# Optimization experiments

Hardware: AMD Instinct MI355X
Metric: run time of the kernel (lower is better)

## Reference

```python
import jax, jax.numpy as jnp
import numpy as np

D_MODEL = 1024


def bitlinear(x, weight):
    # ternary quantization with straight-through estimator; forward value is w_q*scale
    scale = jnp.clip(jnp.mean(jnp.abs(weight), axis=1, keepdims=True), 1e-5, None)
    w_q = jnp.clip(jnp.round(weight / scale), -1.0, 1.0)
    w = weight + jax.lax.stop_gradient(w_q * scale - weight)
    return x @ w.T


def rmsnorm(x, w, eps=1e-6):
    return x * jax.lax.rsqrt(jnp.mean(x * x, axis=-1, keepdims=True) + eps) * w


def setup_inputs() -> dict:
    key = jax.random.key(0)
    ks = jax.random.split(key, 6)
    D = D_MODEL
    std = np.sqrt(2.0 / D)  # kaiming_normal fan_out
    return {
        "x": jax.random.normal(ks[0], (4, 4096, D), dtype=jnp.float32),
        "Wr": jax.random.normal(ks[1], (D, D), dtype=jnp.float32) * std,
        "Wk": jax.random.normal(ks[2], (D, D), dtype=jnp.float32) * std,
        "Wv": jax.random.normal(ks[3], (D, D), dtype=jnp.float32) * std,
        "Wo": jax.random.normal(ks[4], (D, D), dtype=jnp.float32) * std,
        "decay": jnp.ones((D,), dtype=jnp.float32) * 0.99,
        "ln_w": jnp.ones((D,), dtype=jnp.float32),
    }


def reference(x, Wr, Wk, Wv, Wo, decay, ln_w):
    B, T, D = x.shape
    r = jax.nn.sigmoid(bitlinear(x, Wr))
    k = bitlinear(x, Wk)
    v = bitlinear(x, Wv)
    dec = jax.nn.sigmoid(decay)                              # [D]
    kv = k * v                                               # [B,T,D]
    positions = jnp.arange(T, dtype=x.dtype)                 # [T]
    log_decay = jnp.log(jnp.clip(dec, 1e-7, None))           # [D]
    scale = jnp.exp(positions[:, None] * log_decay[None, :])  # [T,D]
    scaled = kv / jnp.clip(scale, 1e-10, None)[None]         # [B,T,D]
    cum = jnp.cumsum(scaled, axis=1)                         # [B,T,D]
    state = cum * scale[None]                                # [B,T,D]
    return bitlinear(rmsnorm(r * state, ln_w), Wo)
```

## Files before the change

### kernel.cpp

```cpp
#include <hip/hip_runtime.h>

typedef unsigned short u16;
typedef __attribute__((ext_vector_type(8))) short bf16x8;
typedef __attribute__((ext_vector_type(4))) float f32x4;
typedef __attribute__((ext_vector_type(4))) unsigned short u16x4;

#define DM 1024

__device__ __forceinline__ float bf2f(u16 u){
  union { unsigned int i; float f; } v; v.i = ((unsigned int)u)<<16; return v.f;
}
__device__ __forceinline__ u16 f2bf(float f){
  unsigned int x = __float_as_uint(f);
  return (u16)((x + 0x7FFFu + ((x>>16)&1u)) >> 16);
}

__global__ __launch_bounds__(256)
void quantize_w(const float* __restrict__ W0, const float* __restrict__ W1,
                const float* __restrict__ W2, const float* __restrict__ W3,
                u16* __restrict__ wq, float* __restrict__ wsc)
{
  const int gr   = blockIdx.x*4 + (threadIdx.x>>6);
  const int lane = threadIdx.x & 63;
  const int mat  = gr >> 10, row = gr & 1023;
  const float* W = (mat==0)?W0:(mat==1)?W1:(mat==2)?W2:W3;
  const float* wr = W + (size_t)row*DM;
  float4 v[4]; float s = 0.f;
  #pragma unroll
  for (int c=0;c<4;c++){
    v[c] = *(const float4*)&wr[c*256 + lane*4];
    s += fabsf(v[c].x)+fabsf(v[c].y)+fabsf(v[c].z)+fabsf(v[c].w);
  }
  #pragma unroll
  for (int off=32; off; off>>=1) s += __shfl_down(s, off);
  s = __shfl(s, 0);
  const float scale = fmaxf(s*(1.f/1024.f), 1e-5f);
  if (lane==0) wsc[gr] = scale;
  u16* wo = wq + (size_t)gr*DM;
  #pragma unroll
  for (int c=0;c<4;c++){
    u16x4 q;
    q[0] = f2bf(fminf(fmaxf(rintf(v[c].x/scale),-1.f),1.f));
    q[1] = f2bf(fminf(fmaxf(rintf(v[c].y/scale),-1.f),1.f));
    q[2] = f2bf(fminf(fmaxf(rintf(v[c].z/scale),-1.f),1.f));
    q[3] = f2bf(fminf(fmaxf(rintf(v[c].w/scale),-1.f),1.f));
    *(u16x4*)&wo[c*256 + lane*4] = q;
  }
}

__global__ void cvt_x(const float* __restrict__ x, u16* __restrict__ xb){
  const int i = (blockIdx.x*256 + threadIdx.x)*4;
  float4 v = *(const float4*)&x[i];
  u16x4 o; o[0]=f2bf(v.x); o[1]=f2bf(v.y); o[2]=f2bf(v.z); o[3]=f2bf(v.w);
  *(u16x4*)&xb[i] = o;
}


#define SB0 __builtin_amdgcn_sched_barrier(0)
#define WL4  do{ asm volatile("s_waitcnt lgkmcnt(4)" ::: "memory"); SB0; }while(0)
#define WL12 do{ asm volatile("s_waitcnt lgkmcnt(12)" ::: "memory"); SB0; }while(0)
#define WL0  do{ asm volatile("s_waitcnt lgkmcnt(0)" ::: "memory"); SB0; }while(0)
#define VM4  do{ asm volatile("s_waitcnt vmcnt(4)" ::: "memory"); SB0; }while(0)
#define VM0  do{ asm volatile("s_waitcnt vmcnt(0)" ::: "memory"); SB0; }while(0)
#define BARR do{ SB0; __builtin_amdgcn_s_barrier(); SB0; }while(0)

#define STG(gB, off, T, Q, buf) \
  __builtin_amdgcn_global_load_lds( \
    (const __attribute__((address_space(1))) void*)((const char*)(gB) + (off) + (Q)*131072 + (T)*128), \
    (__attribute__((address_space(3))) void*)((char*)(buf) + ldst + (Q)*8192), 16, 0, 0)

#define RD(base, off) (*(const bf16x8*)((const char*)(base) + (off)))

#define MFMA16(AF, B, MI) \
  __builtin_amdgcn_s_setprio(1); \
  _Pragma("unroll") \
  for (int ni=0; ni<4; ++ni){ \
    acc[MI][ni]   = __builtin_amdgcn_mfma_f32_16x16x32_bf16(AF[0], B[ni],   acc[MI][ni],   0,0,0); \
    acc[MI][ni]   = __builtin_amdgcn_mfma_f32_16x16x32_bf16(AF[1], B[4+ni], acc[MI][ni],   0,0,0); \
    acc[MI+1][ni] = __builtin_amdgcn_mfma_f32_16x16x32_bf16(AF[2], B[ni],   acc[MI+1][ni], 0,0,0); \
    acc[MI+1][ni] = __builtin_amdgcn_mfma_f32_16x16x32_bf16(AF[3], B[4+ni], acc[MI+1][ni], 0,0,0); \
  } \
  __builtin_amdgcn_s_setprio(0)

#define TILE(T, C, BCUR, BNXT) { \
  const char* la  = (const char*)sA[C]; \
  const char* lnA = (const char*)sA[(C)^1]; \
  const char* lnB = (const char*)sB[(C)^1]; \
   \
  ay[0]=RD(la, arow+2*2048+koff0); ay[1]=RD(la, arow+2*2048+koff1); \
  ay[2]=RD(la, arow+3*2048+koff0); ay[3]=RD(la, arow+3*2048+koff1); \
  if ((T)+1<nt){ STG(Ag, aoff, (T)+1, 0, sA[(C)^1]); STG(Ag, aoff, (T)+1, 1, sA[(C)^1]); \
                 STG(Ag, aoff, (T)+1, 2, sA[(C)^1]); STG(Ag, aoff, (T)+1, 3, sA[(C)^1]); } \
  WL4; MFMA16(ax, BCUR, 0); BARR; \
   \
  ax[0]=RD(la, arow+4*2048+koff0); ax[1]=RD(la, arow+4*2048+koff1); \
  ax[2]=RD(la, arow+5*2048+koff0); ax[3]=RD(la, arow+5*2048+koff1); \
  if ((T)+2<nt){ STG(Bg, boff, (T)+2, 0, sB[C]); STG(Bg, boff, (T)+2, 1, sB[C]); } \
  WL4; MFMA16(ay, BCUR, 2); BARR; \
   \
  ay[0]=RD(la, arow+6*2048+koff0); ay[1]=RD(la, arow+6*2048+koff1); \
  ay[2]=RD(la, arow+7*2048+koff0); ay[3]=RD(la, arow+7*2048+koff1); \
  if ((T)+2<nt){ STG(Bg, boff, (T)+2, 2, sB[C]); STG(Bg, boff, (T)+2, 3, sB[C]); } \
  WL4; MFMA16(ax, BCUR, 4); SB0; \
  if ((T)==nt-2) { VM0; } else if ((T)<nt-2) { VM4; } \
  BARR; \
   \
  if ((T)<nt-1){ \
    BNXT[0]=RD(lnB, brow+0*2048+koff0); BNXT[1]=RD(lnB, brow+1*2048+koff0); \
    BNXT[2]=RD(lnB, brow+2*2048+koff0); BNXT[3]=RD(lnB, brow+3*2048+koff0); \
    BNXT[4]=RD(lnB, brow+0*2048+koff1); BNXT[5]=RD(lnB, brow+1*2048+koff1); \
    BNXT[6]=RD(lnB, brow+2*2048+koff1); BNXT[7]=RD(lnB, brow+3*2048+koff1); \
    ax[0]=RD(lnA, arow+0*2048+koff0); ax[1]=RD(lnA, arow+0*2048+koff1); \
    ax[2]=RD(lnA, arow+1*2048+koff0); ax[3]=RD(lnA, arow+1*2048+koff1); \
    WL12; \
  } else { WL0; } \
  MFMA16(ay, BCUR, 6); BARR; \
}

template<int MODE>
__global__ __launch_bounds__(512, 2)
void gemm_p(const u16* __restrict__ Ag, const u16* __restrict__ Bg,
            const float* __restrict__ bscale,
            u16* __restrict__ o_r, u16* __restrict__ o_k, u16* __restrict__ o_v,
            float* __restrict__ o_f)
{
  __shared__ u16 sA[2][256*64];
  __shared__ u16 sB[2][256*64];
  const int tid = threadIdx.x, wave = tid>>6, lane = tid&63;
  const int lr = lane&15, lg = lane>>4;
  const int wm = wave>>2, wn = wave&3;
  const int bm0 = blockIdx.x*256, bn0 = blockIdx.y*256;
  constexpr int nt = 16;

  const int r8   = lane>>3;
  const int scol = ((lane&7)<<4) ^ (r8<<4);
  const size_t aoff = (size_t)(bm0 + wave*8 + r8)*2048 + scol;
  const size_t boff = (size_t)(bn0 + wave*8 + r8)*2048 + scol;
  const int ldst = wave*1024;
  const int S = (lr&7)<<4;
  const int koff0 = (0  + (lg<<4)) ^ S;
  const int koff1 = (64 + (lg<<4)) ^ S;
  const int arow = (wm*128 + lr)*128;
  const int brow = (wn*64  + lr)*128;

  f32x4 acc[8][4];
  #pragma unroll
  for (int i=0;i<8;i++)
    #pragma unroll
    for (int j=0;j<4;j++) acc[i][j] = (f32x4){0.f,0.f,0.f,0.f};

  bf16x8 bc[8], bn2[8], ax[4], ay[4];

  #pragma unroll
  for (int q=0;q<4;q++){ STG(Ag, aoff, 0, q, sA[0]); STG(Bg, boff, 0, q, sB[0]); }
  #pragma unroll
  for (int q=0;q<4;q++){ STG(Bg, boff, 1, q, sB[1]); }
  VM4;
  BARR;
  {
    const char* la0 = (const char*)sA[0];
    const char* lb0 = (const char*)sB[0];
    bc[0]=RD(lb0, brow+0*2048+koff0); bc[1]=RD(lb0, brow+1*2048+koff0);
    bc[2]=RD(lb0, brow+2*2048+koff0); bc[3]=RD(lb0, brow+3*2048+koff0);
    bc[4]=RD(lb0, brow+0*2048+koff1); bc[5]=RD(lb0, brow+1*2048+koff1);
    bc[6]=RD(lb0, brow+2*2048+koff1); bc[7]=RD(lb0, brow+3*2048+koff1);
    ax[0]=RD(la0, arow+0*2048+koff0); ax[1]=RD(la0, arow+0*2048+koff1);
    ax[2]=RD(la0, arow+1*2048+koff0); ax[3]=RD(la0, arow+1*2048+koff1);
  }
  for (int tp=0; tp<nt; tp+=2){
    TILE(tp,   0, bc, bn2)
    TILE(tp+1, 1, bn2, bc)
  }

  #pragma unroll
  for (int mi=0; mi<8; ++mi){
    #pragma unroll
    for (int ni=0; ni<4; ++ni){
      const int col = bn0 + wn*64 + ni*16 + lr;
      const float sc = bscale[col];
      const int rowb = bm0 + wm*128 + mi*16 + lg*4;
      const f32x4 a = acc[mi][ni];
      if (MODE==0){
        const int seg = col>>10, d = col&1023;
        #pragma unroll
        for (int r2=0;r2<4;r2++){
          const size_t o = (size_t)(rowb+r2)*DM + d;
          const float val = a[r2]*sc;
          if (seg==0)      o_r[o] = f2bf(1.f/(1.f+expf(-val)));
          else if (seg==1) o_k[o] = f2bf(val);
          else             o_v[o] = f2bf(val);
        }
      } else {
        #pragma unroll
        for (int r2=0;r2<4;r2++)
          o_f[(size_t)(rowb+r2)*DM + col] = a[r2]*sc;
      }
    }
  }
}

__global__ __launch_bounds__(256)
void kv_phase1(const u16* __restrict__ kb, const u16* __restrict__ vb,
               const float* __restrict__ decay, float* __restrict__ part)
{
  const int c = blockIdx.x & 127, b = blockIdx.x >> 7;
  const int d0 = threadIdx.x*4;
  float ld[4]; f32x4 sum = {0.f,0.f,0.f,0.f};
  #pragma unroll
  for (int j=0;j<4;j++){
    const float dec = 1.f/(1.f+expf(-decay[d0+j]));
    ld[j] = logf(fmaxf(dec, 1e-7f));
  }
  for (int t=c*32; t<c*32+32; ++t){
    const size_t base = ((size_t)(b*4096 + t))*DM + d0;
    const u16x4 k4 = *(const u16x4*)&kb[base];
    const u16x4 v4 = *(const u16x4*)&vb[base];
    const float tf = (float)t;
    #pragma unroll
    for (int j=0;j<4;j++){
      const float e = expf(tf*ld[j]);
      sum[j] += bf2f(k4[j])*bf2f(v4[j]) / fmaxf(e, 1e-10f);
    }
  }
  *(f32x4*)&part[((size_t)(b*128+c))*DM + d0] = sum;
}

__global__ void chunk_prefix(float* __restrict__ part){
  const int g = blockIdx.x*256 + threadIdx.x;
  const int b = g >> 8, d0 = (g & 255)*4;
  f32x4 run = {0.f,0.f,0.f,0.f};
  for (int c8=0; c8<128; c8+=8){
    f32x4 v[8];
    #pragma unroll
    for (int i=0;i<8;i++)
      v[i] = *(const f32x4*)&part[((size_t)(b*128+c8+i))*DM + d0];
    #pragma unroll
    for (int i=0;i<8;i++){
      const f32x4 tmp = v[i];
      *(f32x4*)&part[((size_t)(b*128+c8+i))*DM + d0] = run;
      run += tmp;
    }
  }
}

__global__ __launch_bounds__(256)
void scan_norm(const u16* __restrict__ kb, const u16* __restrict__ vb,
               const u16* __restrict__ rbuf, const float* __restrict__ part,
               const float* __restrict__ decay, const float* __restrict__ lnw,
               u16* __restrict__ yn)
{
  const int c = blockIdx.x & 127, b = blockIdx.x >> 7;
  const int tid = threadIdx.x, lane = tid&63, wave = tid>>6;
  const int d0 = tid*4;
  __shared__ float red[2][4];
  f32x4 run = *(const f32x4*)&part[((size_t)(b*128+c))*DM + d0];
  float ld[4], lw[4];
  #pragma unroll
  for (int j=0;j<4;j++){
    const float dec = 1.f/(1.f+expf(-decay[d0+j]));
    ld[j] = logf(fmaxf(dec, 1e-7f));
    lw[j] = lnw[d0+j];
  }
  for (int t=c*32; t<c*32+32; ++t){
    const size_t base = ((size_t)(b*4096+t))*DM + d0;
    const u16x4 k4 = *(const u16x4*)&kb[base];
    const u16x4 v4 = *(const u16x4*)&vb[base];
    const u16x4 r4 = *(const u16x4*)&rbuf[base];
    const float tf = (float)t;
    float y[4]; float ss = 0.f;
    #pragma unroll
    for (int j=0;j<4;j++){
      const float e = expf(tf*ld[j]);
      run[j] += bf2f(k4[j])*bf2f(v4[j]) / fmaxf(e, 1e-10f);
      const float st = run[j]*e;
      y[j] = bf2f(r4[j])*st;
      ss += y[j]*y[j];
    }
    #pragma unroll
    for (int off=32; off; off>>=1) ss += __shfl_down(ss, off);
    if (lane==0) red[t&1][wave] = ss;
    __builtin_amdgcn_s_barrier();
    const float tot = (red[t&1][0]+red[t&1][1])+(red[t&1][2]+red[t&1][3]);
    const float rs = 1.f/sqrtf(tot*(1.f/1024.f) + 1e-6f);
    u16x4 o;
    #pragma unroll
    for (int j=0;j<4;j++) o[j] = f2bf(y[j]*rs*lw[j]);
    *(u16x4*)&yn[base] = o;
  }
}

extern "C" void kernel_launch(void* const* d_in, const int* in_sizes, int n_in,
                              void* d_out, int out_size, void* d_ws, size_t ws_size,
                              hipStream_t stream)
{
  (void)in_sizes; (void)n_in; (void)out_size; (void)ws_size;
  const float* x    = (const float*)d_in[0];
  const float* Wr   = (const float*)d_in[1];
  const float* Wk   = (const float*)d_in[2];
  const float* Wv   = (const float*)d_in[3];
  const float* Wo   = (const float*)d_in[4];
  const float* dec  = (const float*)d_in[5];
  const float* lnw  = (const float*)d_in[6];

  char* ws = (char*)d_ws;
  u16*   wq     = (u16*)(ws + 0);
  float* wsc    = (float*)(ws + 8388608);
  u16*   rbuf   = (u16*)(ws + 8404992);
  u16*   kbuf   = (u16*)(ws + 41959424);
  u16*   vbuf   = (u16*)(ws + 75513856);
  float* part   = (float*)(ws + 109068288);
  u16*   xb     = (u16*)(ws + 111165440);
  u16*   yn     = xb;

  quantize_w<<<1024, 256, 0, stream>>>(Wr, Wk, Wv, Wo, wq, wsc);
  cvt_x<<<16384, 256, 0, stream>>>(x, xb);
  gemm_p<0><<<dim3(64,12), 512, 0, stream>>>(xb, wq, wsc, rbuf, kbuf, vbuf, nullptr);
  kv_phase1<<<512, 256, 0, stream>>>(kbuf, vbuf, dec, part);
  chunk_prefix<<<4, 256, 0, stream>>>(part);
  scan_norm<<<512, 256, 0, stream>>>(kbuf, vbuf, rbuf, part, dec, lnw, yn);
  gemm_p<1><<<dim3(64,4), 512, 0, stream>>>(yn, wq + 3*1024*1024, wsc + 3072,
                                            nullptr, nullptr, nullptr, (float*)d_out);
}
```

Baseline: 250.6 us.

## Switch GEMM inner loop to 32x32x16 bf16 MFMA with restructured LDS reads

Replaces the 16x16x32 MFMA tiling with 32x32x16 MFMA instructions, so each wave now holds 4x2 32x32 accumulator blocks. B fragments are re-read from LDS each tile instead of being prefetched into double-buffered registers, and A fragments rotate between two register sets. The main loop is split into a steady-state body without bounds checks plus two peeled tail tiles, and the epilogue is remapped to the 32x32 output layout. Larger MFMAs need fewer instructions and LDS fragment reads per FLOP, but B reads are no longer hidden behind the previous tile's compute, and the epilogue writes use a more scattered row pattern.

```diff
diff --git a/kernel.cpp b/kernel.cpp
--- a/kernel.cpp
+++ b/kernel.cpp
@@ -3,6 +3,7 @@
 typedef unsigned short u16;
 typedef __attribute__((ext_vector_type(8))) short bf16x8;
 typedef __attribute__((ext_vector_type(4))) float f32x4;
+typedef __attribute__((ext_vector_type(16))) float f32x16;
 typedef __attribute__((ext_vector_type(4))) unsigned short u16x4;
 
 #define DM 1024
@@ -58,7 +59,6 @@
 
 #define SB0 __builtin_amdgcn_sched_barrier(0)
 #define WL4  do{ asm volatile("s_waitcnt lgkmcnt(4)" ::: "memory"); SB0; }while(0)
-#define WL12 do{ asm volatile("s_waitcnt lgkmcnt(12)" ::: "memory"); SB0; }while(0)
 #define WL0  do{ asm volatile("s_waitcnt lgkmcnt(0)" ::: "memory"); SB0; }while(0)
 #define VM4  do{ asm volatile("s_waitcnt vmcnt(4)" ::: "memory"); SB0; }while(0)
 #define VM0  do{ asm volatile("s_waitcnt vmcnt(0)" ::: "memory"); SB0; }while(0)
@@ -66,55 +66,48 @@
 
 #define STG(gB, off, T, Q, buf) \
   __builtin_amdgcn_global_load_lds( \
-    (const __attribute__((address_space(1))) void*)((const char*)(gB) + (off) + (Q)*131072 + (T)*128), \
+    (const __attribute__((address_space(1))) void*)((const char*)(gB) + (off) + (Q)*131072 + (size_t)(T)*128), \
     (__attribute__((address_space(3))) void*)((char*)(buf) + ldst + (Q)*8192), 16, 0, 0)
 
 #define RD(base, off) (*(const bf16x8*)((const char*)(base) + (off)))
 
-#define MFMA16(AF, B, MI) \
+#define RDA4(DST, BASE, ROWOFF) \
+  DST[0]=RD(BASE,(ROWOFF)+koff0); DST[1]=RD(BASE,(ROWOFF)+koff1); \
+  DST[2]=RD(BASE,(ROWOFF)+koff2); DST[3]=RD(BASE,(ROWOFF)+koff3);
+
+#define MFMA8(AF, MI) \
   __builtin_amdgcn_s_setprio(1); \
   _Pragma("unroll") \
-  for (int ni=0; ni<4; ++ni){ \
-    acc[MI][ni]   = __builtin_amdgcn_mfma_f32_16x16x32_bf16(AF[0], B[ni],   acc[MI][ni],   0,0,0); \
-    acc[MI][ni]   = __builtin_amdgcn_mfma_f32_16x16x32_bf16(AF[1], B[4+ni], acc[MI][ni],   0,0,0); \
-    acc[MI+1][ni] = __builtin_amdgcn_mfma_f32_16x16x32_bf16(AF[2], B[ni],   acc[MI+1][ni], 0,0,0); \
-    acc[MI+1][ni] = __builtin_amdgcn_mfma_f32_16x16x32_bf16(AF[3], B[4+ni], acc[MI+1][ni], 0,0,0); \
+  for (int kk=0; kk<4; ++kk){ \
+    acc[MI][0] = __builtin_amdgcn_mfma_f32_32x32x16_bf16(AF[kk], bF[0][kk], acc[MI][0], 0,0,0); \
+    acc[MI][1] = __builtin_amdgcn_mfma_f32_32x32x16_bf16(AF[kk], bF[1][kk], acc[MI][1], 0,0,0); \
   } \
   __builtin_amdgcn_s_setprio(0)
 
-#define TILE(T, C, BCUR, BNXT) { \
+#define TILE(T, C, FULL) { \
   const char* la  = (const char*)sA[C]; \
+  const char* lb  = (const char*)sB[C]; \
   const char* lnA = (const char*)sA[(C)^1]; \
-  const char* lnB = (const char*)sB[(C)^1]; \
    \
-  ay[0]=RD(la, arow+2*2048+koff0); ay[1]=RD(la, arow+2*2048+koff1); \
-  ay[2]=RD(la, arow+3*2048+koff0); ay[3]=RD(la, arow+3*2048+koff1); \
-  if ((T)+1<nt){ STG(Ag, aoff, (T)+1, 0, sA[(C)^1]); STG(Ag, aoff, (T)+1, 1, sA[(C)^1]); \
-                 STG(Ag, aoff, (T)+1, 2, sA[(C)^1]); STG(Ag, aoff, (T)+1, 3, sA[(C)^1]); } \
-  WL4; MFMA16(ax, BCUR, 0); BARR; \
+  RDA4(bF[0], lb, brow) \
+  RDA4(bF[1], lb, brow+4096) \
+  RDA4(aA, la, arow+4096) \
+  if (FULL || (T)+1<nt){ STG(Ag,aoff,(T)+1,0,sA[(C)^1]); STG(Ag,aoff,(T)+1,1,sA[(C)^1]); \
+                         STG(Ag,aoff,(T)+1,2,sA[(C)^1]); STG(Ag,aoff,(T)+1,3,sA[(C)^1]); } \
+  WL4; MFMA8(aB, 0); BARR; \
    \
-  ax[0]=RD(la, arow+4*2048+koff0); ax[1]=RD(la, arow+4*2048+koff1); \
-  ax[2]=RD(la, arow+5*2048+koff0); ax[3]=RD(la, arow+5*2048+koff1); \
-  if ((T)+2<nt){ STG(Bg, boff, (T)+2, 0, sB[C]); STG(Bg, boff, (T)+2, 1, sB[C]); } \
-  WL4; MFMA16(ay, BCUR, 2); BARR; \
+  RDA4(aB, la, arow+2*4096) \
+  if (FULL || (T)+2<nt){ STG(Bg,boff,(T)+2,0,sB[C]); STG(Bg,boff,(T)+2,1,sB[C]); } \
+  WL4; MFMA8(aA, 1); BARR; \
    \
-  ay[0]=RD(la, arow+6*2048+koff0); ay[1]=RD(la, arow+6*2048+koff1); \
-  ay[2]=RD(la, arow+7*2048+koff0); ay[3]=RD(la, arow+7*2048+koff1); \
-  if ((T)+2<nt){ STG(Bg, boff, (T)+2, 2, sB[C]); STG(Bg, boff, (T)+2, 3, sB[C]); } \
-  WL4; MFMA16(ax, BCUR, 4); SB0; \
-  if ((T)==nt-2) { VM0; } else if ((T)<nt-2) { VM4; } \
+  RDA4(aA, la, arow+3*4096) \
+  if (FULL || (T)+2<nt){ STG(Bg,boff,(T)+2,2,sB[C]); STG(Bg,boff,(T)+2,3,sB[C]); } \
+  WL4; MFMA8(aB, 2); SB0; \
+  if (FULL || (T)<nt-2) { VM4; } else if ((T)==nt-2) { VM0; } \
   BARR; \
    \
-  if ((T)<nt-1){ \
-    BNXT[0]=RD(lnB, brow+0*2048+koff0); BNXT[1]=RD(lnB, brow+1*2048+koff0); \
-    BNXT[2]=RD(lnB, brow+2*2048+koff0); BNXT[3]=RD(lnB, brow+3*2048+koff0); \
-    BNXT[4]=RD(lnB, brow+0*2048+koff1); BNXT[5]=RD(lnB, brow+1*2048+koff1); \
-    BNXT[6]=RD(lnB, brow+2*2048+koff1); BNXT[7]=RD(lnB, brow+3*2048+koff1); \
-    ax[0]=RD(lnA, arow+0*2048+koff0); ax[1]=RD(lnA, arow+0*2048+koff1); \
-    ax[2]=RD(lnA, arow+1*2048+koff0); ax[3]=RD(lnA, arow+1*2048+koff1); \
-    WL12; \
-  } else { WL0; } \
-  MFMA16(ay, BCUR, 6); BARR; \
+  if (FULL || (T)<nt-1){ RDA4(aB, lnA, arow) WL4; } else { WL0; } \
+  MFMA8(aA, 3); BARR; \
 }
 
 template<int MODE>
@@ -127,7 +120,7 @@
   __shared__ u16 sA[2][256*64];
   __shared__ u16 sB[2][256*64];
   const int tid = threadIdx.x, wave = tid>>6, lane = tid&63;
-  const int lr = lane&15, lg = lane>>4;
+  const int ll = lane&31, lh = lane>>5;
   const int wm = wave>>2, wn = wave&3;
   const int bm0 = blockIdx.x*256, bn0 = blockIdx.y*256;
   constexpr int nt = 16;
@@ -137,19 +130,22 @@
   const size_t aoff = (size_t)(bm0 + wave*8 + r8)*2048 + scol;
   const size_t boff = (size_t)(bn0 + wave*8 + r8)*2048 + scol;
   const int ldst = wave*1024;
-  const int S = (lr&7)<<4;
-  const int koff0 = (0  + (lg<<4)) ^ S;
-  const int koff1 = (64 + (lg<<4)) ^ S;
-  const int arow = (wm*128 + lr)*128;
-  const int brow = (wn*64  + lr)*128;
-
-  f32x4 acc[8][4];
-  #pragma unroll
-  for (int i=0;i<8;i++)
-    #pragma unroll
-    for (int j=0;j<4;j++) acc[i][j] = (f32x4){0.f,0.f,0.f,0.f};
-
-  bf16x8 bc[8], bn2[8], ax[4], ay[4];
+  const int S = (ll&7)<<4;
+  const int koff0 = (0*32 + (lh<<4)) ^ S;
+  const int koff1 = (1*32 + (lh<<4)) ^ S;
+  const int koff2 = (2*32 + (lh<<4)) ^ S;
+  const int koff3 = (3*32 + (lh<<4)) ^ S;
+  const int arow = (wm*128 + ll)*128;
+  const int brow = (wn*64  + ll)*128;
+
+  f32x16 acc[4][2];
+  #pragma unroll
+  for (int i=0;i<4;i++)
+    #pragma unroll
+    for (int j=0;j<2;j++)
+      acc[i][j] = (f32x16){0,0,0,0,0,0,0,0,0,0,0,0,0,0,0,0};
+
+  bf16x8 bF[2][4], aA[4], aB[4];
 
   #pragma unroll
   for (int q=0;q<4;q++){ STG(Ag, aoff, 0, q, sA[0]); STG(Bg, boff, 0, q, sB[0]); }
@@ -157,43 +153,40 @@
   for (int q=0;q<4;q++){ STG(Bg, boff, 1, q, sB[1]); }
   VM4;
   BARR;
-  {
-    const char* la0 = (const char*)sA[0];
-    const char* lb0 = (const char*)sB[0];
-    bc[0]=RD(lb0, brow+0*2048+koff0); bc[1]=RD(lb0, brow+1*2048+koff0);
-    bc[2]=RD(lb0, brow+2*2048+koff0); bc[3]=RD(lb0, brow+3*2048+koff0);
-    bc[4]=RD(lb0, brow+0*2048+koff1); bc[5]=RD(lb0, brow+1*2048+koff1);
-    bc[6]=RD(lb0, brow+2*2048+koff1); bc[7]=RD(lb0, brow+3*2048+koff1);
-    ax[0]=RD(la0, arow+0*2048+koff0); ax[1]=RD(la0, arow+0*2048+koff1);
-    ax[2]=RD(la0, arow+1*2048+koff0); ax[3]=RD(la0, arow+1*2048+koff1);
-  }
-  for (int tp=0; tp<nt; tp+=2){
-    TILE(tp,   0, bc, bn2)
-    TILE(tp+1, 1, bn2, bc)
-  }
-
-  #pragma unroll
-  for (int mi=0; mi<8; ++mi){
-    #pragma unroll
-    for (int ni=0; ni<4; ++ni){
-      const int col = bn0 + wn*64 + ni*16 + lr;
+  RDA4(aB, (const char*)sA[0], arow)
+
+  for (int tp=0; tp<nt-2; tp+=2){
+    TILE(tp,   0, true)
+    TILE(tp+1, 1, true)
+  }
+  TILE(14, 0, false)
+  TILE(15, 1, false)
+
+  #pragma unroll
+  for (int m=0; m<4; ++m){
+    #pragma unroll
+    for (int n=0; n<2; ++n){
+      const int col = bn0 + wn*64 + n*32 + ll;
       const float sc = bscale[col];
-      const int rowb = bm0 + wm*128 + mi*16 + lg*4;
-      const f32x4 a = acc[mi][ni];
+      const int rowb = bm0 + wm*128 + m*32 + lh*4;
+      const f32x16 a = acc[m][n];
       if (MODE==0){
         const int seg = col>>10, d = col&1023;
         #pragma unroll
-        for (int r2=0;r2<4;r2++){
-          const size_t o = (size_t)(rowb+r2)*DM + d;
-          const float val = a[r2]*sc;
+        for (int r=0;r<16;r++){
+          const int row = rowb + (r&3) + 8*(r>>2);
+          const float val = a[r]*sc;
+          const size_t o = (size_t)row*DM + d;
           if (seg==0)      o_r[o] = f2bf(1.f/(1.f+expf(-val)));
           else if (seg==1) o_k[o] = f2bf(val);
           else             o_v[o] = f2bf(val);
         }
       } else {
         #pragma unroll
-        for (int r2=0;r2<4;r2++)
-          o_f[(size_t)(rowb+r2)*DM + col] = a[r2]*sc;
+        for (int r=0;r<16;r++){
+          const int row = rowb + (r&3) + 8*(r>>2);
+          o_f[(size_t)row*DM + col] = a[r]*sc;
+        }
       }
     }
   }
```

Measured after the change: 466.1 us. 1.86x slower.

## Replace 256x256 GEMM with 128x128 tiles loading B directly into registers

Applied to the files above, without the earlier changes.

Replaces the 512-thread 256x256-tile GEMM and its hand-scheduled software pipeline with a 256-thread 128x128-tile kernel. Only A is staged through LDS, double-buffered. B fragments are read straight from global memory into registers, skipping LDS staging for the weights. The aim is more resident blocks per CU (launch bounds 256,3), a larger grid and a simpler schedule. In exchange, data reuse per tile is lower, more global traffic goes to the weights, and the deeper interleaving of LDS reads with MFMA is lost.

```diff
diff --git a/kernel.cpp b/kernel.cpp
--- a/kernel.cpp
+++ b/kernel.cpp
@@ -57,128 +57,97 @@
 
 
 #define SB0 __builtin_amdgcn_sched_barrier(0)
-#define WL4  do{ asm volatile("s_waitcnt lgkmcnt(4)" ::: "memory"); SB0; }while(0)
-#define WL12 do{ asm volatile("s_waitcnt lgkmcnt(12)" ::: "memory"); SB0; }while(0)
-#define WL0  do{ asm volatile("s_waitcnt lgkmcnt(0)" ::: "memory"); SB0; }while(0)
-#define VM4  do{ asm volatile("s_waitcnt vmcnt(4)" ::: "memory"); SB0; }while(0)
-#define VM0  do{ asm volatile("s_waitcnt vmcnt(0)" ::: "memory"); SB0; }while(0)
 #define BARR do{ SB0; __builtin_amdgcn_s_barrier(); SB0; }while(0)
-
-#define STG(gB, off, T, Q, buf) \
-  __builtin_amdgcn_global_load_lds( \
-    (const __attribute__((address_space(1))) void*)((const char*)(gB) + (off) + (Q)*131072 + (T)*128), \
-    (__attribute__((address_space(3))) void*)((char*)(buf) + ldst + (Q)*8192), 16, 0, 0)
-
 #define RD(base, off) (*(const bf16x8*)((const char*)(base) + (off)))
 
-#define MFMA16(AF, B, MI) \
+#define ASTG(T, BUF) { _Pragma("unroll") \
+  for (int q=0;q<4;q++) \
+    __builtin_amdgcn_global_load_lds( \
+      (const __attribute__((address_space(1))) void*)(asrc[q] + (size_t)(T)*128), \
+      (__attribute__((address_space(3))) void*)((char*)(BUF) + ldst + q*4096), 16, 0, 0); }
+
+#define GBODY(T, C, DO_STAGE, WA, WB, TRAIL) { \
+  bf16x8 b0[4], b1[4], a0[4], a1[4]; \
+  _Pragma("unroll") \
+  for (int n=0;n<4;n++){ b0[n]=RD(bptr[n], (size_t)(T)*128); \
+                         b1[n]=RD(bptr[n], (size_t)(T)*128+64); } \
+  SB0; \
+  if (DO_STAGE) ASTG((T)+1, sA[(C)^1]); \
+  SB0; \
+  asm volatile("s_waitcnt vmcnt(" #WA ")" ::: "memory"); \
+  __builtin_amdgcn_s_barrier(); \
+  SB0; \
+  _Pragma("unroll") \
+  for (int m=0;m<4;m++){ a0[m]=RD((const char*)sA[C], arow + m*2048 + koff0); \
+                         a1[m]=RD((const char*)sA[C], arow + m*2048 + koff1); } \
+  SB0; \
+  asm volatile("s_waitcnt vmcnt(" #WB ") lgkmcnt(0)" ::: "memory"); \
+  SB0; \
   __builtin_amdgcn_s_setprio(1); \
   _Pragma("unroll") \
-  for (int ni=0; ni<4; ++ni){ \
-    acc[MI][ni]   = __builtin_amdgcn_mfma_f32_16x16x32_bf16(AF[0], B[ni],   acc[MI][ni],   0,0,0); \
-    acc[MI][ni]   = __builtin_amdgcn_mfma_f32_16x16x32_bf16(AF[1], B[4+ni], acc[MI][ni],   0,0,0); \
-    acc[MI+1][ni] = __builtin_amdgcn_mfma_f32_16x16x32_bf16(AF[2], B[ni],   acc[MI+1][ni], 0,0,0); \
-    acc[MI+1][ni] = __builtin_amdgcn_mfma_f32_16x16x32_bf16(AF[3], B[4+ni], acc[MI+1][ni], 0,0,0); \
-  } \
-  __builtin_amdgcn_s_setprio(0)
-
-#define TILE(T, C, BCUR, BNXT) { \
-  const char* la  = (const char*)sA[C]; \
-  const char* lnA = (const char*)sA[(C)^1]; \
-  const char* lnB = (const char*)sB[(C)^1]; \
-   \
-  ay[0]=RD(la, arow+2*2048+koff0); ay[1]=RD(la, arow+2*2048+koff1); \
-  ay[2]=RD(la, arow+3*2048+koff0); ay[3]=RD(la, arow+3*2048+koff1); \
-  if ((T)+1<nt){ STG(Ag, aoff, (T)+1, 0, sA[(C)^1]); STG(Ag, aoff, (T)+1, 1, sA[(C)^1]); \
-                 STG(Ag, aoff, (T)+1, 2, sA[(C)^1]); STG(Ag, aoff, (T)+1, 3, sA[(C)^1]); } \
-  WL4; MFMA16(ax, BCUR, 0); BARR; \
-   \
-  ax[0]=RD(la, arow+4*2048+koff0); ax[1]=RD(la, arow+4*2048+koff1); \
-  ax[2]=RD(la, arow+5*2048+koff0); ax[3]=RD(la, arow+5*2048+koff1); \
-  if ((T)+2<nt){ STG(Bg, boff, (T)+2, 0, sB[C]); STG(Bg, boff, (T)+2, 1, sB[C]); } \
-  WL4; MFMA16(ay, BCUR, 2); BARR; \
-   \
-  ay[0]=RD(la, arow+6*2048+koff0); ay[1]=RD(la, arow+6*2048+koff1); \
-  ay[2]=RD(la, arow+7*2048+koff0); ay[3]=RD(la, arow+7*2048+koff1); \
-  if ((T)+2<nt){ STG(Bg, boff, (T)+2, 2, sB[C]); STG(Bg, boff, (T)+2, 3, sB[C]); } \
-  WL4; MFMA16(ax, BCUR, 4); SB0; \
-  if ((T)==nt-2) { VM0; } else if ((T)<nt-2) { VM4; } \
-  BARR; \
-   \
-  if ((T)<nt-1){ \
-    BNXT[0]=RD(lnB, brow+0*2048+koff0); BNXT[1]=RD(lnB, brow+1*2048+koff0); \
-    BNXT[2]=RD(lnB, brow+2*2048+koff0); BNXT[3]=RD(lnB, brow+3*2048+koff0); \
-    BNXT[4]=RD(lnB, brow+0*2048+koff1); BNXT[5]=RD(lnB, brow+1*2048+koff1); \
-    BNXT[6]=RD(lnB, brow+2*2048+koff1); BNXT[7]=RD(lnB, brow+3*2048+koff1); \
-    ax[0]=RD(lnA, arow+0*2048+koff0); ax[1]=RD(lnA, arow+0*2048+koff1); \
-    ax[2]=RD(lnA, arow+1*2048+koff0); ax[3]=RD(lnA, arow+1*2048+koff1); \
-    WL12; \
-  } else { WL0; } \
-  MFMA16(ay, BCUR, 6); BARR; \
+  for (int m=0;m<4;m++){ \
+    _Pragma("unroll") \
+    for (int n=0;n<4;n++){ \
+      acc[m][n] = __builtin_amdgcn_mfma_f32_16x16x32_bf16(a0[m], b0[n], acc[m][n], 0,0,0); \
+      acc[m][n] = __builtin_amdgcn_mfma_f32_16x16x32_bf16(a1[m], b1[n], acc[m][n], 0,0,0); \
+    } } \
+  __builtin_amdgcn_s_setprio(0); \
+  if (TRAIL) BARR; \
 }
 
 template<int MODE>
-__global__ __launch_bounds__(512, 2)
-void gemm_p(const u16* __restrict__ Ag, const u16* __restrict__ Bg,
+__global__ __launch_bounds__(256, 3)
+void gemm_t(const u16* __restrict__ Ag, const u16* __restrict__ Bg,
             const float* __restrict__ bscale,
             u16* __restrict__ o_r, u16* __restrict__ o_k, u16* __restrict__ o_v,
             float* __restrict__ o_f)
 {
-  __shared__ u16 sA[2][256*64];
-  __shared__ u16 sB[2][256*64];
+  __shared__ u16 sA[2][128*64];
   const int tid = threadIdx.x, wave = tid>>6, lane = tid&63;
   const int lr = lane&15, lg = lane>>4;
-  const int wm = wave>>2, wn = wave&3;
-  const int bm0 = blockIdx.x*256, bn0 = blockIdx.y*256;
+  const int wm = wave>>1, wn = wave&1;
+  const int bm0 = blockIdx.x*128, bn0 = blockIdx.y*128;
   constexpr int nt = 16;
 
   const int r8   = lane>>3;
   const int scol = ((lane&7)<<4) ^ (r8<<4);
-  const size_t aoff = (size_t)(bm0 + wave*8 + r8)*2048 + scol;
-  const size_t boff = (size_t)(bn0 + wave*8 + r8)*2048 + scol;
+  const char* asrc[4];
+  #pragma unroll
+  for (int q=0;q<4;q++)
+    asrc[q] = (const char*)Ag + (size_t)(bm0 + q*32 + wave*8 + r8)*2048 + scol;
   const int ldst = wave*1024;
+
+  const char* bptr[4];
+  #pragma unroll
+  for (int n=0;n<4;n++)
+    bptr[n] = (const char*)Bg + (size_t)(bn0 + wn*64 + n*16 + lr)*2048 + lg*16;
+
   const int S = (lr&7)<<4;
-  const int koff0 = (0  + (lg<<4)) ^ S;
+  const int koff0 = (lg<<4) ^ S;
   const int koff1 = (64 + (lg<<4)) ^ S;
-  const int arow = (wm*128 + lr)*128;
-  const int brow = (wn*64  + lr)*128;
-
-  f32x4 acc[8][4];
-  #pragma unroll
-  for (int i=0;i<8;i++)
+  const int arow = (wm*64 + lr)*128;
+
+  f32x4 acc[4][4];
+  #pragma unroll
+  for (int i=0;i<4;i++)
     #pragma unroll
     for (int j=0;j<4;j++) acc[i][j] = (f32x4){0.f,0.f,0.f,0.f};
 
-  bf16x8 bc[8], bn2[8], ax[4], ay[4];
-
-  #pragma unroll
-  for (int q=0;q<4;q++){ STG(Ag, aoff, 0, q, sA[0]); STG(Bg, boff, 0, q, sB[0]); }
-  #pragma unroll
-  for (int q=0;q<4;q++){ STG(Bg, boff, 1, q, sB[1]); }
-  VM4;
-  BARR;
-  {
-    const char* la0 = (const char*)sA[0];
-    const char* lb0 = (const char*)sB[0];
-    bc[0]=RD(lb0, brow+0*2048+koff0); bc[1]=RD(lb0, brow+1*2048+koff0);
-    bc[2]=RD(lb0, brow+2*2048+koff0); bc[3]=RD(lb0, brow+3*2048+koff0);
-    bc[4]=RD(lb0, brow+0*2048+koff1); bc[5]=RD(lb0, brow+1*2048+koff1);
-    bc[6]=RD(lb0, brow+2*2048+koff1); bc[7]=RD(lb0, brow+3*2048+koff1);
-    ax[0]=RD(la0, arow+0*2048+koff0); ax[1]=RD(la0, arow+0*2048+koff1);
-    ax[2]=RD(la0, arow+1*2048+koff0); ax[3]=RD(la0, arow+1*2048+koff1);
-  }
-  for (int tp=0; tp<nt; tp+=2){
-    TILE(tp,   0, bc, bn2)
-    TILE(tp+1, 1, bn2, bc)
-  }
-
-  #pragma unroll
-  for (int mi=0; mi<8; ++mi){
+  ASTG(0, sA[0]);
+
+  for (int t=0; t<nt-1; ++t){
+    const int c = t&1;
+    GBODY(t, c, true, 12, 4, true)
+  }
+  GBODY(nt-1, (nt-1)&1, false, 8, 0, false)
+
+  #pragma unroll
+  for (int mi=0; mi<4; ++mi){
     #pragma unroll
     for (int ni=0; ni<4; ++ni){
       const int col = bn0 + wn*64 + ni*16 + lr;
       const float sc = bscale[col];
-      const int rowb = bm0 + wm*128 + mi*16 + lg*4;
+      const int rowb = bm0 + wm*64 + mi*16 + lg*4;
       const f32x4 a = acc[mi][ni];
       if (MODE==0){
         const int seg = col>>10, d = col&1023;
@@ -314,10 +283,10 @@
 
   quantize_w<<<1024, 256, 0, stream>>>(Wr, Wk, Wv, Wo, wq, wsc);
   cvt_x<<<16384, 256, 0, stream>>>(x, xb);
-  gemm_p<0><<<dim3(64,12), 512, 0, stream>>>(xb, wq, wsc, rbuf, kbuf, vbuf, nullptr);
+  gemm_t<0><<<dim3(128,24), 256, 0, stream>>>(xb, wq, wsc, rbuf, kbuf, vbuf, nullptr);
   kv_phase1<<<512, 256, 0, stream>>>(kbuf, vbuf, dec, part);
   chunk_prefix<<<4, 256, 0, stream>>>(part);
   scan_norm<<<512, 256, 0, stream>>>(kbuf, vbuf, rbuf, part, dec, lnw, yn);
-  gemm_p<1><<<dim3(64,4), 512, 0, stream>>>(yn, wq + 3*1024*1024, wsc + 3072,
-                                            nullptr, nullptr, nullptr, (float*)d_out);
-}
+  gemm_t<1><<<dim3(128,8), 256, 0, stream>>>(yn, wq + 3*1024*1024, wsc + 3072,
+                                             nullptr, nullptr, nullptr, (float*)d_out);
+}
```

Result: slower. 385.9 us (+54.0%).

## Interleave Wk/Wv rows so GEMM epilogue emits k*v product directly

Applied to the files above, without the earlier changes.

Quantized Wk and Wv rows are interleaved so adjacent output columns of the QKV GEMM hold k and v for the same channel. The epilogue multiplies them with a lane shuffle and writes a single bf16 kv buffer instead of separate k and v buffers. The scan kernels then read one tensor instead of two. This cuts global write and read traffic, but half the lanes stay idle during the kv store, the stores are strided, and k*v is now rounded to bf16 as a product rather than as separate factors.

```diff
diff --git a/kernel.cpp b/kernel.cpp
--- a/kernel.cpp
+++ b/kernel.cpp
@@ -22,8 +22,10 @@
 {
   const int gr   = blockIdx.x*4 + (threadIdx.x>>6);
   const int lane = threadIdx.x & 63;
-  const int mat  = gr >> 10, row = gr & 1023;
-  const float* W = (mat==0)?W0:(mat==1)?W1:(mat==2)?W2:W3;
+  const float* W; int row;
+  if (gr < 1024)      { W = W0; row = gr; }
+  else if (gr < 3072) { row = (gr-1024)>>1; W = (gr&1) ? W2 : W1; }
+  else                { W = W3; row = gr-3072; }
   const float* wr = W + (size_t)row*DM;
   float4 v[4]; float s = 0.f;
   #pragma unroll
@@ -66,7 +68,7 @@
 
 #define STG(gB, off, T, Q, buf) \
   __builtin_amdgcn_global_load_lds( \
-    (const __attribute__((address_space(1))) void*)((const char*)(gB) + (off) + (Q)*131072 + (T)*128), \
+    (const __attribute__((address_space(1))) void*)((const char*)(gB) + (off) + (Q)*131072 + (size_t)(T)*128), \
     (__attribute__((address_space(3))) void*)((char*)(buf) + ldst + (Q)*8192), 16, 0, 0)
 
 #define RD(base, off) (*(const bf16x8*)((const char*)(base) + (off)))
@@ -121,7 +123,7 @@
 __global__ __launch_bounds__(512, 2)
 void gemm_p(const u16* __restrict__ Ag, const u16* __restrict__ Bg,
             const float* __restrict__ bscale,
-            u16* __restrict__ o_r, u16* __restrict__ o_k, u16* __restrict__ o_v,
+            u16* __restrict__ o_r, u16* __restrict__ o_kv,
             float* __restrict__ o_f)
 {
   __shared__ u16 sA[2][256*64];
@@ -181,14 +183,21 @@
       const int rowb = bm0 + wm*128 + mi*16 + lg*4;
       const f32x4 a = acc[mi][ni];
       if (MODE==0){
-        const int seg = col>>10, d = col&1023;
-        #pragma unroll
-        for (int r2=0;r2<4;r2++){
-          const size_t o = (size_t)(rowb+r2)*DM + d;
-          const float val = a[r2]*sc;
-          if (seg==0)      o_r[o] = f2bf(1.f/(1.f+expf(-val)));
-          else if (seg==1) o_k[o] = f2bf(val);
-          else             o_v[o] = f2bf(val);
+        if (bn0 < 1024){
+          #pragma unroll
+          for (int r2=0;r2<4;r2++){
+            const float val = a[r2]*sc;
+            o_r[(size_t)(rowb+r2)*DM + col] = f2bf(1.f/(1.f+expf(-val)));
+          }
+        } else {
+          const int dv = (col - 1024) >> 1;
+          #pragma unroll
+          for (int r2=0;r2<4;r2++){
+            const float val = a[r2]*sc;
+            const float pr  = val * __shfl_xor(val, 1);
+            if (!(lr & 1))
+              o_kv[(size_t)(rowb+r2)*DM + dv] = f2bf(pr);
+          }
         }
       } else {
         #pragma unroll
@@ -200,8 +209,8 @@
 }
 
 __global__ __launch_bounds__(256)
-void kv_phase1(const u16* __restrict__ kb, const u16* __restrict__ vb,
-               const float* __restrict__ decay, float* __restrict__ part)
+void kv_phase1(const u16* __restrict__ kv, const float* __restrict__ decay,
+               float* __restrict__ part)
 {
   const int c = blockIdx.x & 127, b = blockIdx.x >> 7;
   const int d0 = threadIdx.x*4;
@@ -213,13 +222,12 @@
   }
   for (int t=c*32; t<c*32+32; ++t){
     const size_t base = ((size_t)(b*4096 + t))*DM + d0;
-    const u16x4 k4 = *(const u16x4*)&kb[base];
-    const u16x4 v4 = *(const u16x4*)&vb[base];
+    const u16x4 p4 = *(const u16x4*)&kv[base];
     const float tf = (float)t;
     #pragma unroll
     for (int j=0;j<4;j++){
       const float e = expf(tf*ld[j]);
-      sum[j] += bf2f(k4[j])*bf2f(v4[j]) / fmaxf(e, 1e-10f);
+      sum[j] += bf2f(p4[j]) / fmaxf(e, 1e-10f);
     }
   }
   *(f32x4*)&part[((size_t)(b*128+c))*DM + d0] = sum;
@@ -244,10 +252,9 @@
 }
 
 __global__ __launch_bounds__(256)
-void scan_norm(const u16* __restrict__ kb, const u16* __restrict__ vb,
-               const u16* __restrict__ rbuf, const float* __restrict__ part,
-               const float* __restrict__ decay, const float* __restrict__ lnw,
-               u16* __restrict__ yn)
+void scan_norm(const u16* __restrict__ kv, const u16* __restrict__ rbuf,
+               const float* __restrict__ part, const float* __restrict__ decay,
+               const float* __restrict__ lnw, u16* __restrict__ yn)
 {
   const int c = blockIdx.x & 127, b = blockIdx.x >> 7;
   const int tid = threadIdx.x, lane = tid&63, wave = tid>>6;
@@ -263,15 +270,14 @@
   }
   for (int t=c*32; t<c*32+32; ++t){
     const size_t base = ((size_t)(b*4096+t))*DM + d0;
-    const u16x4 k4 = *(const u16x4*)&kb[base];
-    const u16x4 v4 = *(const u16x4*)&vb[base];
+    const u16x4 p4 = *(const u16x4*)&kv[base];
     const u16x4 r4 = *(const u16x4*)&rbuf[base];
     const float tf = (float)t;
     float y[4]; float ss = 0.f;
     #pragma unroll
     for (int j=0;j<4;j++){
       const float e = expf(tf*ld[j]);
-      run[j] += bf2f(k4[j])*bf2f(v4[j]) / fmaxf(e, 1e-10f);
+      run[j] += bf2f(p4[j]) / fmaxf(e, 1e-10f);
       const float st = run[j]*e;
       y[j] = bf2f(r4[j])*st;
       ss += y[j]*y[j];
@@ -306,18 +312,17 @@
   u16*   wq     = (u16*)(ws + 0);
   float* wsc    = (float*)(ws + 8388608);
   u16*   rbuf   = (u16*)(ws + 8404992);
-  u16*   kbuf   = (u16*)(ws + 41959424);
-  u16*   vbuf   = (u16*)(ws + 75513856);
-  float* part   = (float*)(ws + 109068288);
-  u16*   xb     = (u16*)(ws + 111165440);
-  u16*   yn     = xb;
+  u16*   kvbuf  = (u16*)(ws + 41959424);
+  float* part   = (float*)(ws + 75513856);
+  u16*   xb     = (u16*)(ws + 77611008);
+  u16*   yn     = (u16*)(ws + 111165440);
 
   quantize_w<<<1024, 256, 0, stream>>>(Wr, Wk, Wv, Wo, wq, wsc);
   cvt_x<<<16384, 256, 0, stream>>>(x, xb);
-  gemm_p<0><<<dim3(64,12), 512, 0, stream>>>(xb, wq, wsc, rbuf, kbuf, vbuf, nullptr);
-  kv_phase1<<<512, 256, 0, stream>>>(kbuf, vbuf, dec, part);
+  gemm_p<0><<<dim3(64,12), 512, 0, stream>>>(xb, wq, wsc, rbuf, kvbuf, nullptr);
+  kv_phase1<<<512, 256, 0, stream>>>(kvbuf, dec, part);
   chunk_prefix<<<4, 256, 0, stream>>>(part);
-  scan_norm<<<512, 256, 0, stream>>>(kbuf, vbuf, rbuf, part, dec, lnw, yn);
+  scan_norm<<<512, 256, 0, stream>>>(kvbuf, rbuf, part, dec, lnw, yn);
   gemm_p<1><<<dim3(64,4), 512, 0, stream>>>(yn, wq + 3*1024*1024, wsc + 3072,
-                                            nullptr, nullptr, nullptr, (float*)d_out);
-}
+                                            nullptr, nullptr, (float*)d_out);
+}
```

Result: faster. 244.0 us (-2.6%).
